# Kernel tuning notes

Hardware: AMD Instinct MI355X
Metric: run time of the kernel (lower is better)

Reference implementation:

```python
import jax, jax.numpy as jnp
import numpy as np
import math

D_MODEL = 1024
N_HEADS = 16
D_K = D_MODEL // N_HEADS
FFN = 4096
B, S = 4, 1024
EPS = 1e-5


def setup_inputs() -> dict:
    key = jax.random.key(0)
    ks = jax.random.split(key, 24)
    sd = 0.02
    def w(k, shape):
        return jax.random.normal(k, shape, dtype=jnp.float32) * sd
    inp = {
        'x': jax.random.normal(ks[0], (B, S, D_MODEL), dtype=jnp.float32),
        'enc': jax.random.normal(ks[1], (B, S, D_MODEL), dtype=jnp.float32),
        'mask': jnp.tril(jnp.ones((S, S), dtype=jnp.int32)),  # causal look-ahead mask
        # stacked per-head projections [H, d_model, d_k], biases [H, d_k]
        'Wq_self': w(ks[2], (N_HEADS, D_MODEL, D_K)), 'bq_self': w(ks[3], (N_HEADS, D_K)),
        'Wk_self': w(ks[4], (N_HEADS, D_MODEL, D_K)), 'bk_self': w(ks[5], (N_HEADS, D_K)),
        'Wv_self': w(ks[6], (N_HEADS, D_MODEL, D_K)), 'bv_self': w(ks[7], (N_HEADS, D_K)),
        'Wq_x': w(ks[8], (N_HEADS, D_MODEL, D_K)), 'bq_x': w(ks[9], (N_HEADS, D_K)),
        'Wk_x': w(ks[10], (N_HEADS, D_MODEL, D_K)), 'bk_x': w(ks[11], (N_HEADS, D_K)),
        'Wv_x': w(ks[12], (N_HEADS, D_MODEL, D_K)), 'bv_x': w(ks[13], (N_HEADS, D_K)),
        # W_O is SHARED between self- and cross-attention (as in the torch code)
        'Wo': w(ks[14], (D_MODEL, D_MODEL)), 'bo': w(ks[15], (D_MODEL,)),
        'W1': w(ks[16], (D_MODEL, FFN)), 'b1': w(ks[17], (FFN,)),
        'W2': w(ks[18], (FFN, D_MODEL)), 'b2': w(ks[19], (D_MODEL,)),
        'g1': jnp.ones((D_MODEL,), jnp.float32), 'be1': jnp.zeros((D_MODEL,), jnp.float32),
        'g2': jnp.ones((D_MODEL,), jnp.float32), 'be2': jnp.zeros((D_MODEL,), jnp.float32),
        'g3': jnp.ones((D_MODEL,), jnp.float32), 'be3': jnp.zeros((D_MODEL,), jnp.float32),
    }
    return inp


def _layernorm(x, g, b):
    mu = jnp.mean(x, axis=-1, keepdims=True)
    d = x - mu
    var = jnp.mean(d * d, axis=-1, keepdims=True)
    return d * jax.lax.rsqrt(var + EPS) * g + b


def _mha(xq, xkv, Wq, bq, Wk, bk, Wv, bv, mask):
    # batched equivalent of the per-head Python loop
    q = jnp.einsum('bsd,hdk->bhsk', xq, Wq) + bq[None, :, None, :]
    k = jnp.einsum('btd,hdk->bhtk', xkv, Wk) + bk[None, :, None, :]
    v = jnp.einsum('btd,hdk->bhtk', xkv, Wv) + bv[None, :, None, :]
    scores = jnp.einsum('bhsk,bhtk->bhst', q, k) / math.sqrt(D_K)
    if mask is not None:
        scores = jnp.where(mask[None, None] == 0, -jnp.inf, scores)
    attn = jax.nn.softmax(scores, axis=-1)
    z = jnp.einsum('bhst,bhtk->bhsk', attn, v)
    # concat heads along last dim (head i occupies slice i, matching torch.cat)
    b_, h_, s_, k_ = z.shape
    return jnp.transpose(z, (0, 2, 1, 3)).reshape(b_, s_, h_ * k_)


def reference(x, enc, mask, Wq_self, bq_self, Wk_self, bk_self, Wv_self, bv_self,
              Wq_x, bq_x, Wk_x, bk_x, Wv_x, bv_x, Wo, bo, W1, b1, W2, b2,
              g1, be1, g2, be2, g3, be3):
    sa = _mha(x, x, Wq_self, bq_self, Wk_self, bk_self, Wv_self, bv_self, mask)
    x1 = _layernorm(x + sa @ Wo + bo, g1, be1)
    ca = _mha(x1, enc, Wq_x, bq_x, Wk_x, bk_x, Wv_x, bv_x, None)
    x2 = _layernorm(x1 + ca @ Wo + bo, g2, be2)
    ffn = jax.nn.relu(x2 @ W1 + b1) @ W2 + b2
    return _layernorm(x2 + ffn, g3, be3)
```

## Files before the change

### kernel.cpp

```cpp
#include <hip/hip_runtime.h>
#include <cstdint>

typedef __bf16 bf16_t;
typedef bf16_t bf16x8 __attribute__((ext_vector_type(8)));
typedef bf16_t bf16x4 __attribute__((ext_vector_type(4)));
typedef float  f32x4  __attribute__((ext_vector_type(4)));

#define DEVI static __device__ __forceinline__

DEVI void async_ld16(const bf16_t* g, bf16_t* l) {
  __builtin_amdgcn_global_load_lds((const __attribute__((address_space(1))) void*)g,
                                   (__attribute__((address_space(3))) void*)l, 16, 0, 0);
}

struct PrepArgs {
  const float *WqS, *WkS, *WvS, *WqX, *WkX, *WvX, *Wo, *W1, *W2, *x, *enc;
  const float *bqS, *bkS, *bvS, *bkX, *bvX;
  bf16_t *WqkvST, *WqXT, *WkvXT, *WoT, *W1T, *W2T, *xb, *encb;
  float *bqkv, *bkvx;
};

__global__ __launch_bounds__(256)
void k_prep(PrepArgs a)
{
  __shared__ float tile[32][33];
  const int blk = blockIdx.x, tid = threadIdx.x;
  const int tx = tid & 31, ty = tid >> 5;

  const float* src = nullptr;
  bf16_t* dst = nullptr;
  int srcLd = 0, dstLd = 0, m0 = 0, n0 = 0;
  bool do_tr = false;

  if (blk < 6144) {
    int j = blk >> 10, q = blk & 1023;
    src = j == 0 ? a.WqS : j == 1 ? a.WkS : j == 2 ? a.WvS : j == 3 ? a.WqX : j == 4 ? a.WkX : a.WvX;
    dst = j == 0 ? a.WqkvST : j == 1 ? a.WqkvST + 1048576 : j == 2 ? a.WqkvST + 2097152
        : j == 3 ? a.WqXT : j == 4 ? a.WkvXT : a.WkvXT + 1048576;
    int batch = q >> 6, rem = q & 63;
    src += (long)batch * 65536; dst += (long)batch * 65536;
    srcLd = 64; dstLd = 1024;
    n0 = (rem & 1) * 32; m0 = (rem >> 1) * 32;
    do_tr = true;
  } else if (blk < 7168) {
    int q = blk - 6144;
    src = a.Wo; dst = a.WoT; srcLd = 1024; dstLd = 1024;
    m0 = (q >> 5) * 32; n0 = (q & 31) * 32; do_tr = true;
  } else if (blk < 11264) {
    int q = blk - 7168;
    src = a.W1; dst = a.W1T; srcLd = 4096; dstLd = 1024;
    m0 = (q >> 7) * 32; n0 = (q & 127) * 32; do_tr = true;
  } else if (blk < 15360) {
    int q = blk - 11264;
    src = a.W2; dst = a.W2T; srcLd = 1024; dstLd = 4096;
    m0 = (q >> 5) * 32; n0 = (q & 31) * 32; do_tr = true;
  } else if (blk < 16384) {
    long base = (long)(blk - 15360) * 4096 + tid * 4;
#pragma unroll
    for (int u = 0; u < 4; u++) {
      float4 v = *(const float4*)(a.x + base + u * 1024);
      bf16x4 o; o[0] = (bf16_t)v.x; o[1] = (bf16_t)v.y; o[2] = (bf16_t)v.z; o[3] = (bf16_t)v.w;
      *(bf16x4*)(a.xb + base + u * 1024) = o;
    }
    return;
  } else if (blk < 17408) {
    long base = (long)(blk - 16384) * 4096 + tid * 4;
#pragma unroll
    for (int u = 0; u < 4; u++) {
      float4 v = *(const float4*)(a.enc + base + u * 1024);
      bf16x4 o; o[0] = (bf16_t)v.x; o[1] = (bf16_t)v.y; o[2] = (bf16_t)v.z; o[3] = (bf16_t)v.w;
      *(bf16x4*)(a.encb + base + u * 1024) = o;
    }
    return;
  } else {
    int gi = (blk - 17408) * 1024 + tid * 4;
#pragma unroll
    for (int j = 0; j < 4; j++) {
      int i = gi + j;
      if (i < 1024)      a.bqkv[i] = a.bqS[i];
      else if (i < 2048) a.bqkv[i] = a.bkS[i - 1024];
      else if (i < 3072) a.bqkv[i] = a.bvS[i - 2048];
      else if (i < 4096) a.bkvx[i - 3072] = a.bkX[i - 3072];
      else if (i < 5120) a.bkvx[i - 3072] = a.bvX[i - 4096];
    }
    return;
  }

  if (do_tr) {
#pragma unroll
    for (int i = 0; i < 4; i++)
      tile[ty + i * 8][tx] = src[(long)(m0 + ty + i * 8) * srcLd + n0 + tx];
    __syncthreads();
#pragma unroll
    for (int i = 0; i < 4; i++)
      dst[(long)(n0 + ty + i * 8) * dstLd + m0 + tx] = (bf16_t)tile[tx][ty + i * 8];
  }
}

template<int OUT_MODE, int RELU>
__global__ __launch_bounds__(256, 2)
void k_gemm(const bf16_t* __restrict__ A, int lda,
            const bf16_t* __restrict__ Bt, int ldb,
            const float* __restrict__ bias,
            bf16_t* __restrict__ C, int ldc,
            bf16_t* __restrict__ p0, bf16_t* __restrict__ p1,
            bf16_t* __restrict__ p2, bf16_t* __restrict__ p3,
            int Ktot, int nx)
{
  __shared__ bf16_t As[2][128 * 32];
  __shared__ bf16_t Bs[2][128 * 32];
  const int tid  = threadIdx.x;
  const int wave = tid >> 6, lane = tid & 63;
  const int quad = lane >> 4, m16 = lane & 15;

  int lin = blockIdx.x;
  int perx = gridDim.x >> 3;
  int t = (lin & 7) * perx + (lin >> 3);
  const int bcol = (t % nx) * 128, brow = (t / nx) * 128;
  const int wr = (wave >> 1) * 64, wc = (wave & 1) * 64;

  const int Kper = Ktot / gridDim.z;
  const int k0 = blockIdx.z * Kper;

  f32x4 acc[4][4];
#pragma unroll
  for (int i = 0; i < 4; i++)
#pragma unroll
    for (int j = 0; j < 4; j++) acc[i][j] = (f32x4){0.f, 0.f, 0.f, 0.f};

  auto stage = [&](int kt, int buf) {
#pragma unroll
    for (int i = 0; i < 2; i++) {
      int rg = wave * 2 + i;
      async_ld16(A  + (long)(brow + rg * 16 + m16) * lda + kt + quad * 8, As[buf] + rg * 512);
      async_ld16(Bt + (long)(bcol + rg * 16 + m16) * ldb + kt + quad * 8, Bs[buf] + rg * 512);
    }
  };

  stage(k0, 0);
  __syncthreads();

  const int nIter = Kper >> 5;
  for (int it = 0; it < nIter; it++) {
    const int cur = it & 1;
    if (it + 1 < nIter) stage(k0 + (it + 1) * 32, cur ^ 1);

    bf16x8 af[4], bfr[4];
#pragma unroll
    for (int tt = 0; tt < 4; tt++) {
      af[tt]  = *(const bf16x8*)(As[cur] + ((wr + tt * 16) >> 4) * 512 + quad * 128 + m16 * 8);
      bfr[tt] = *(const bf16x8*)(Bs[cur] + ((wc + tt * 16) >> 4) * 512 + quad * 128 + m16 * 8);
    }
#pragma unroll
    for (int i = 0; i < 4; i++)
#pragma unroll
      for (int j = 0; j < 4; j++)
        acc[i][j] = __builtin_amdgcn_mfma_f32_16x16x32_bf16(af[i], bfr[j], acc[i][j], 0, 0, 0);

    __syncthreads();
  }

  if (OUT_MODE == 1) {
    bf16_t* P = blockIdx.z == 0 ? p0 : blockIdx.z == 1 ? p1 : blockIdx.z == 2 ? p2 : p3;
#pragma unroll
    for (int i = 0; i < 4; i++)
#pragma unroll
      for (int j = 0; j < 4; j++) {
        int col = bcol + wc + j * 16 + m16;
#pragma unroll
        for (int r = 0; r < 4; r++) {
          int row = brow + wr + i * 16 + quad * 4 + r;
          P[(long)row * ldc + col] = (bf16_t)acc[i][j][r];
        }
      }
  } else {
#pragma unroll
    for (int i = 0; i < 4; i++)
#pragma unroll
      for (int j = 0; j < 4; j++) {
        int col = bcol + wc + j * 16 + m16;
        float bv = bias[col];
#pragma unroll
        for (int r = 0; r < 4; r++) {
          int row = brow + wr + i * 16 + quad * 4 + r;
          float v = acc[i][j][r] + bv;
          if (RELU) v = v > 0.f ? v : 0.f;
          C[(long)row * ldc + col] = (bf16_t)v;
        }
      }
  }
}

__global__ __launch_bounds__(256, 2)
void k_gemm_qkv(const bf16_t* __restrict__ A0, const bf16_t* __restrict__ B0,
                const float* __restrict__ bias0, bf16_t* __restrict__ C0, bf16_t* __restrict__ Vt0,
                const bf16_t* __restrict__ A1, const bf16_t* __restrict__ B1,
                const float* __restrict__ bias1, bf16_t* __restrict__ C1, bf16_t* __restrict__ Vt1)
{
  __shared__ bf16_t As[2][128 * 32];
  __shared__ bf16_t Bs[2][128 * 32];
  const int tid  = threadIdx.x;
  const int wave = tid >> 6, lane = tid & 63;
  const int quad = lane >> 4, m16 = lane & 15;

  int lin = blockIdx.x;
  int perx = gridDim.x >> 3;
  int t = (lin & 7) * perx + (lin >> 3);

  const bf16_t *A, *Bt; const float* bias; bf16_t *C, *Vt;
  int nx, ldc, voff, qthresh, tl;
  if (t < 768) {
    A = A0; Bt = B0; bias = bias0; C = C0; Vt = Vt0;
    nx = 24; ldc = 2048; voff = 2048; qthresh = 1024; tl = t;
  } else {
    A = A1; Bt = B1; bias = bias1; C = C1; Vt = Vt1;
    nx = 16; ldc = 1024; voff = 1024; qthresh = 0; tl = t - 768;
  }
  const int bcol = (tl % nx) * 128, brow = (tl / nx) * 128;
  const int wr = (wave >> 1) * 64, wc = (wave & 1) * 64;

  f32x4 acc[4][4];
#pragma unroll
  for (int i = 0; i < 4; i++)
#pragma unroll
    for (int j = 0; j < 4; j++) acc[i][j] = (f32x4){0.f, 0.f, 0.f, 0.f};

  auto stage = [&](int kt, int buf) {
#pragma unroll
    for (int i = 0; i < 2; i++) {
      int rg = wave * 2 + i;
      async_ld16(A  + (long)(brow + rg * 16 + m16) * 1024 + kt + quad * 8, As[buf] + rg * 512);
      async_ld16(Bt + (long)(bcol + rg * 16 + m16) * 1024 + kt + quad * 8, Bs[buf] + rg * 512);
    }
  };

  stage(0, 0);
  __syncthreads();

  for (int it = 0; it < 32; it++) {
    const int cur = it & 1;
    if (it + 1 < 32) stage((it + 1) * 32, cur ^ 1);

    bf16x8 af[4], bfr[4];
#pragma unroll
    for (int tt = 0; tt < 4; tt++) {
      af[tt]  = *(const bf16x8*)(As[cur] + ((wr + tt * 16) >> 4) * 512 + quad * 128 + m16 * 8);
      bfr[tt] = *(const bf16x8*)(Bs[cur] + ((wc + tt * 16) >> 4) * 512 + quad * 128 + m16 * 8);
    }
#pragma unroll
    for (int i = 0; i < 4; i++)
#pragma unroll
      for (int j = 0; j < 4; j++)
        acc[i][j] = __builtin_amdgcn_mfma_f32_16x16x32_bf16(af[i], bfr[j], acc[i][j], 0, 0, 0);

    __syncthreads();
  }

#pragma unroll
  for (int i = 0; i < 4; i++)
#pragma unroll
    for (int j = 0; j < 4; j++) {
      int col = bcol + wc + j * 16 + m16;
      float bv = bias[col];
      if (col >= voff) {
        int hh = (col - voff) >> 6, dd = col & 63;
        int row0 = brow + wr + i * 16 + quad * 4;
        int bb = row0 >> 10, seq = row0 & 1023;
        bf16x4 pk;
#pragma unroll
        for (int r = 0; r < 4; r++) pk[r] = (bf16_t)(acc[i][j][r] + bv);
        *(bf16x4*)(Vt + (long)(bb * 16 + hh) * 65536 + dd * 1024 + seq) = pk;
      } else {
        float sc = (col < qthresh) ? 0.125f : 1.0f;
#pragma unroll
        for (int r = 0; r < 4; r++) {
          int row = brow + wr + i * 16 + quad * 4 + r;
          C[(long)row * ldc + col] = (bf16_t)((acc[i][j][r] + bv) * sc);
        }
      }
    }
}

template<int LN, int RESID, int OUTF, int OUTB, int QS>
__global__ __launch_bounds__(256)
void k_reduce4(const bf16_t* __restrict__ p0, const bf16_t* __restrict__ p1,
               const bf16_t* __restrict__ p2, const bf16_t* __restrict__ p3,
               const float* __restrict__ bias, const float* __restrict__ resid,
               const float* __restrict__ gamma, const float* __restrict__ beta,
               float* __restrict__ outf, bf16_t* __restrict__ outb)
{
  constexpr int D = 1024;
  __shared__ float red[8];
  int row = blockIdx.x, tid = threadIdx.x;
  long off = (long)row * D + tid * 4;
  bf16x4 a0 = *(const bf16x4*)(p0 + off);
  bf16x4 a1 = *(const bf16x4*)(p1 + off);
  bf16x4 a2 = *(const bf16x4*)(p2 + off);
  bf16x4 a3 = *(const bf16x4*)(p3 + off);
  float4 bb4 = *(const float4*)(bias + tid * 4);
  float4 v;
  v.x = (float)a0[0] + (float)a1[0] + (float)a2[0] + (float)a3[0] + bb4.x;
  v.y = (float)a0[1] + (float)a1[1] + (float)a2[1] + (float)a3[1] + bb4.y;
  v.z = (float)a0[2] + (float)a1[2] + (float)a2[2] + (float)a3[2] + bb4.z;
  v.w = (float)a0[3] + (float)a1[3] + (float)a2[3] + (float)a3[3] + bb4.w;
  if (RESID) {
    float4 q = *(const float4*)(resid + off);
    v.x += q.x; v.y += q.y; v.z += q.z; v.w += q.w;
  }
  float4 y = v;
  if (LN) {
    float s  = v.x + v.y + v.z + v.w;
    float sq = v.x * v.x + v.y * v.y + v.z * v.z + v.w * v.w;
#pragma unroll
    for (int o = 1; o < 64; o <<= 1) {
      s  += __shfl_xor(s, o, 64);
      sq += __shfl_xor(sq, o, 64);
    }
    int wave = tid >> 6, lane = tid & 63;
    if (lane == 0) { red[wave * 2] = s; red[wave * 2 + 1] = sq; }
    __syncthreads();
    float ts = red[0] + red[2] + red[4] + red[6];
    float tq = red[1] + red[3] + red[5] + red[7];
    float mu = ts * (1.f / D);
    float var = tq * (1.f / D) - mu * mu;
    float rstd = rsqrtf(var + 1e-5f);
    float4 g  = *(const float4*)(gamma + tid * 4);
    float4 be = *(const float4*)(beta + tid * 4);
    y.x = (v.x - mu) * rstd * g.x + be.x;
    y.y = (v.y - mu) * rstd * g.y + be.y;
    y.z = (v.z - mu) * rstd * g.z + be.z;
    y.w = (v.w - mu) * rstd * g.w + be.w;
  }
  if (OUTF) *(float4*)(outf + off) = y;
  if (OUTB) {
    if (QS) { y.x *= 0.125f; y.y *= 0.125f; y.z *= 0.125f; y.w *= 0.125f; }
    bf16x4 o;
    o[0] = (bf16_t)y.x; o[1] = (bf16_t)y.y; o[2] = (bf16_t)y.z; o[3] = (bf16_t)y.w;
    *(bf16x4*)(outb + off) = o;
  }
}

template<int CAUSAL>
__global__ __launch_bounds__(256, 2)
void k_attn(const bf16_t* __restrict__ Q, int ldq,
            const bf16_t* __restrict__ Kp, int ldk,
            const bf16_t* __restrict__ Vt,
            bf16_t* __restrict__ O)
{
  constexpr int S = 1024;
  __shared__ bf16_t Kls[2][4096];
  __shared__ bf16_t Vls[2][4096];
  __shared__ bf16_t Pls[4][32 * 72];

  const int tid = threadIdx.x;
  const int wave = tid >> 6, lane = tid & 63;
  const int quad = lane >> 4, m16 = lane & 15;
  const int qt = blockIdx.x, bh = blockIdx.y, b = bh >> 4, h = bh & 15;
  const int qbase = qt * 128 + wave * 32;

  bf16x8 qf[2][2];
#pragma unroll
  for (int rh = 0; rh < 2; rh++) {
    const bf16_t* qp = Q + (long)(b * S + qbase + rh * 16 + m16) * ldq + h * 64 + quad * 8;
    qf[rh][0] = *(const bf16x8*)qp;
    qf[rh][1] = *(const bf16x8*)(qp + 32);
  }

  f32x4 o_acc[2][4];
#pragma unroll
  for (int rh = 0; rh < 2; rh++)
#pragma unroll
    for (int t = 0; t < 4; t++) o_acc[rh][t] = (f32x4){0.f, 0.f, 0.f, 0.f};
  float rsum[2][4];
#pragma unroll
  for (int rh = 0; rh < 2; rh++)
#pragma unroll
    for (int r = 0; r < 4; r++) rsum[rh][r] = 0.f;

  auto stage = [&](int c, int buf) {
#pragma unroll
    for (int i = 0; i < 2; i++) {
      int t2 = wave * 2 + i;
      int rg = t2 & 3, ph = t2 >> 2;
      async_ld16(Kp + (long)(b * S + c * 64 + rg * 16 + m16) * ldk + h * 64 + ph * 32 + quad * 8,
                 Kls[buf] + t2 * 512);
      async_ld16(Vt + (long)bh * 65536 + (rg * 16 + m16) * 1024 + c * 64 + ph * 32 + quad * 8,
                 Vls[buf] + t2 * 512);
    }
  };

  const int nch = CAUSAL ? (2 * qt + 2) : 16;
  stage(0, 0);

  for (int c = 0; c < nch; c++) {
    __syncthreads();
    const int cur = c & 1;
    if (c + 1 < nch) stage(c + 1, cur ^ 1);

    f32x4 s[2][4];
#pragma unroll
    for (int t = 0; t < 4; t++) {
      bf16x8 k0 = *(const bf16x8*)(Kls[cur] + (0 * 4 + t) * 512 + quad * 128 + m16 * 8);
      bf16x8 k1 = *(const bf16x8*)(Kls[cur] + (1 * 4 + t) * 512 + quad * 128 + m16 * 8);
#pragma unroll
      for (int rh = 0; rh < 2; rh++) {
        f32x4 z = (f32x4){0.f, 0.f, 0.f, 0.f};
        z = __builtin_amdgcn_mfma_f32_16x16x32_bf16(qf[rh][0], k0, z, 0, 0, 0);
        z = __builtin_amdgcn_mfma_f32_16x16x32_bf16(qf[rh][1], k1, z, 0, 0, 0);
        s[rh][t] = z;
      }
    }

    bf16_t* pw = Pls[wave];
#pragma unroll
    for (int rh = 0; rh < 2; rh++)
#pragma unroll
      for (int r = 0; r < 4; r++) {
        int qg = qbase + rh * 16 + quad * 4 + r;
#pragma unroll
        for (int t = 0; t < 4; t++) {
          float v = s[rh][t][r];
          float p;
          if (CAUSAL) {
            int kvg = c * 64 + t * 16 + m16;
            p = (kvg <= qg) ? __expf(v) : 0.f;
          } else {
            p = __expf(v);
          }
          rsum[rh][r] += p;
          pw[(rh * 16 + quad * 4 + r) * 72 + t * 16 + m16] = (bf16_t)p;
        }
      }

    bf16x8 pf[2][2];
#pragma unroll
    for (int rh = 0; rh < 2; rh++)
#pragma unroll
      for (int kvh = 0; kvh < 2; kvh++)
        pf[rh][kvh] = *(const bf16x8*)(pw + (rh * 16 + m16) * 72 + kvh * 32 + quad * 8);
#pragma unroll
    for (int t = 0; t < 4; t++) {
      bf16x8 v0 = *(const bf16x8*)(Vls[cur] + (0 * 4 + t) * 512 + quad * 128 + m16 * 8);
      bf16x8 v1 = *(const bf16x8*)(Vls[cur] + (1 * 4 + t) * 512 + quad * 128 + m16 * 8);
#pragma unroll
      for (int rh = 0; rh < 2; rh++) {
        o_acc[rh][t] = __builtin_amdgcn_mfma_f32_16x16x32_bf16(pf[rh][0], v0, o_acc[rh][t], 0, 0, 0);
        o_acc[rh][t] = __builtin_amdgcn_mfma_f32_16x16x32_bf16(pf[rh][1], v1, o_acc[rh][t], 0, 0, 0);
      }
    }
  }

#pragma unroll
  for (int rh = 0; rh < 2; rh++)
#pragma unroll
    for (int r = 0; r < 4; r++) {
      float v = rsum[rh][r];
      v += __shfl_xor(v, 1, 64);
      v += __shfl_xor(v, 2, 64);
      v += __shfl_xor(v, 4, 64);
      v += __shfl_xor(v, 8, 64);
      rsum[rh][r] = 1.f / v;
    }
#pragma unroll
  for (int rh = 0; rh < 2; rh++)
#pragma unroll
    for (int t = 0; t < 4; t++)
#pragma unroll
      for (int r = 0; r < 4; r++) {
        int row = b * S + qbase + rh * 16 + quad * 4 + r;
        int col = h * 64 + t * 16 + m16;
        O[(long)row * 1024 + col] = (bf16_t)(o_acc[rh][t][r] * rsum[rh][r]);
      }
}

extern "C" void kernel_launch(void* const* d_in, const int* in_sizes, int n_in,
                              void* d_out, int out_size, void* d_ws, size_t ws_size,
                              hipStream_t stream)
{
  const float* x   = (const float*)d_in[0];
  const float* enc = (const float*)d_in[1];
  const float* WqS = (const float*)d_in[3];
  const float* bqS = (const float*)d_in[4];
  const float* WkS = (const float*)d_in[5];
  const float* bkS = (const float*)d_in[6];
  const float* WvS = (const float*)d_in[7];
  const float* bvS = (const float*)d_in[8];
  const float* WqX = (const float*)d_in[9];
  const float* bqX = (const float*)d_in[10];
  const float* WkX = (const float*)d_in[11];
  const float* bkX = (const float*)d_in[12];
  const float* WvX = (const float*)d_in[13];
  const float* bvX = (const float*)d_in[14];
  const float* Wo  = (const float*)d_in[15];
  const float* bo  = (const float*)d_in[16];
  const float* W1  = (const float*)d_in[17];
  const float* b1  = (const float*)d_in[18];
  const float* W2  = (const float*)d_in[19];
  const float* b2  = (const float*)d_in[20];
  const float* g1  = (const float*)d_in[21];
  const float* be1 = (const float*)d_in[22];
  const float* g2  = (const float*)d_in[23];
  const float* be2 = (const float*)d_in[24];
  const float* g3  = (const float*)d_in[25];
  const float* be3 = (const float*)d_in[26];

  char* ws = (char*)d_ws;
  const long MBy = 1048576;
  bf16_t* WqkvST = (bf16_t*)(ws + 0 * MBy);
  bf16_t* WqXT   = (bf16_t*)(ws + 6 * MBy);
  bf16_t* WkvXT  = (bf16_t*)(ws + 8 * MBy);
  bf16_t* WoT    = (bf16_t*)(ws + 12 * MBy);
  bf16_t* W1T    = (bf16_t*)(ws + 14 * MBy);
  bf16_t* W2T    = (bf16_t*)(ws + 22 * MBy);
  float*  bqkvS  = (float*)(ws + 30 * MBy);
  float*  bkvX   = (float*)(ws + 30 * MBy + 16384);
  bf16_t* xb     = (bf16_t*)(ws + 31 * MBy);
  bf16_t* Qx     = xb;
  bf16_t* encb   = (bf16_t*)(ws + 39 * MBy);
  float*  x1f    = (float*)(ws + 47 * MBy);
  bf16_t* x1b    = (bf16_t*)(ws + 63 * MBy);
  bf16_t* Z      = (bf16_t*)(ws + 71 * MBy);
  bf16_t* QK     = (bf16_t*)(ws + 79 * MBy);
  bf16_t* Kenc   = (bf16_t*)(ws + 95 * MBy);
  bf16_t* VtS    = (bf16_t*)(ws + 103 * MBy);
  bf16_t* VtX    = (bf16_t*)(ws + 111 * MBy);
  bf16_t* pa0 = (bf16_t*)(ws + 79 * MBy);
  bf16_t* pa1 = (bf16_t*)(ws + 87 * MBy);
  bf16_t* pa2 = (bf16_t*)(ws + 103 * MBy);
  bf16_t* pa3 = (bf16_t*)(ws + 119 * MBy);
  bf16_t* Hbuf = (bf16_t*)(ws + 79 * MBy);
  bf16_t* pf0 = (bf16_t*)(ws + 0 * MBy);
  bf16_t* pf1 = (bf16_t*)(ws + 31 * MBy);
  bf16_t* pf2 = (bf16_t*)(ws + 39 * MBy);
  bf16_t* pf3 = (bf16_t*)(ws + 63 * MBy);

  dim3 tb(256);

  PrepArgs pa;
  pa.WqS = WqS; pa.WkS = WkS; pa.WvS = WvS; pa.WqX = WqX; pa.WkX = WkX; pa.WvX = WvX;
  pa.Wo = Wo; pa.W1 = W1; pa.W2 = W2; pa.x = x; pa.enc = enc;
  pa.bqS = bqS; pa.bkS = bkS; pa.bvS = bvS; pa.bkX = bkX; pa.bvX = bvX;
  pa.WqkvST = WqkvST; pa.WqXT = WqXT; pa.WkvXT = WkvXT; pa.WoT = WoT;
  pa.W1T = W1T; pa.W2T = W2T; pa.xb = xb; pa.encb = encb;
  pa.bqkv = bqkvS; pa.bkvx = bkvX;
  k_prep<<<dim3(17413), tb, 0, stream>>>(pa);

  k_gemm_qkv<<<dim3(1280), tb, 0, stream>>>(
      xb, WqkvST, bqkvS, QK, VtS,
      encb, WkvXT, bkvX, Kenc, VtX);

  k_attn<1><<<dim3(8, 64), tb, 0, stream>>>(QK, 2048, QK + 1024, 2048, VtS, Z);
  k_gemm<1, 0><<<dim3(256, 1, 4), tb, 0, stream>>>(
      Z, 1024, WoT, 1024, nullptr, nullptr, 1024, pa0, pa1, pa2, pa3, 1024, 8);
  k_reduce4<1, 1, 1, 1, 0><<<dim3(4096), tb, 0, stream>>>(
      pa0, pa1, pa2, pa3, bo, x, g1, be1, x1f, x1b);

  k_gemm<1, 0><<<dim3(256, 1, 4), tb, 0, stream>>>(
      x1b, 1024, WqXT, 1024, nullptr, nullptr, 1024, pa0, pa1, pa2, pa3, 1024, 8);
  k_reduce4<0, 0, 0, 1, 1><<<dim3(4096), tb, 0, stream>>>(
      pa0, pa1, pa2, pa3, bqX, nullptr, nullptr, nullptr, nullptr, Qx);
  k_attn<0><<<dim3(8, 64), tb, 0, stream>>>(Qx, 1024, Kenc, 1024, VtX, Z);
  k_gemm<1, 0><<<dim3(256, 1, 4), tb, 0, stream>>>(
      Z, 1024, WoT, 1024, nullptr, nullptr, 1024, pa0, pa1, pa2, pa3, 1024, 8);
  k_reduce4<1, 1, 1, 1, 0><<<dim3(4096), tb, 0, stream>>>(
      pa0, pa1, pa2, pa3, bo, x1f, g2, be2, x1f, x1b);

  k_gemm<0, 1><<<dim3(1024), tb, 0, stream>>>(
      x1b, 1024, W1T, 1024, b1, Hbuf, 4096, nullptr, nullptr, nullptr, nullptr, 1024, 32);
  k_gemm<1, 0><<<dim3(256, 1, 4), tb, 0, stream>>>(
      Hbuf, 4096, W2T, 4096, nullptr, nullptr, 1024, pf0, pf1, pf2, pf3, 4096, 8);
  k_reduce4<1, 1, 1, 0, 0><<<dim3(4096), tb, 0, stream>>>(
      pf0, pf1, pf2, pf3, b2, x1f, g3, be3, (float*)d_out, nullptr);
}
```

Measured before the change: 603.8 us.

## Load GEMM fragments directly from global into registers, dropping LDS staging

Replaces the LDS double-buffered async staging in the GEMM kernels with a shared register double-buffered core. Each lane loads its MFMA fragments straight from global memory, which removes the shared memory and the barriers, and occupancy is raised to 3 blocks per SM. The cost is that waves which previously shared tile data through LDS now each fetch it separately. That roughly doubles L2 traffic and uses strided, less coalesced 16-byte loads per row.

```diff
diff --git a/kernel.cpp b/kernel.cpp
--- a/kernel.cpp
+++ b/kernel.cpp
@@ -97,18 +97,54 @@
   }
 }
 
-template<int OUT_MODE, int RELU>
-__global__ __launch_bounds__(256, 2)
+template<int NITER>
+DEVI void gemm_core(const bf16_t* __restrict__ A, int lda,
+                    const bf16_t* __restrict__ Bt, int ldb,
+                    int brow, int bcol, int k0, int wr, int wc,
+                    int quad, int m16, f32x4 (&acc)[4][4])
+{
+  int aOff[4], bOff[4];
+#pragma unroll
+  for (int i = 0; i < 4; i++) {
+    aOff[i] = (brow + wr + i * 16 + m16) * lda + k0 + quad * 8;
+    bOff[i] = (bcol + wc + i * 16 + m16) * ldb + k0 + quad * 8;
+  }
+
+  bf16x8 aR[2][4], bR[2][4];
+#pragma unroll
+  for (int i = 0; i < 4; i++) {
+    aR[0][i] = *(const bf16x8*)(A + (long)aOff[i]);
+    bR[0][i] = *(const bf16x8*)(Bt + (long)bOff[i]);
+  }
+
+#pragma unroll
+  for (int t = 0; t < NITER; t++) {
+    const int cur = t & 1;
+    if (t + 1 < NITER) {
+#pragma unroll
+      for (int i = 0; i < 4; i++) {
+        aR[cur ^ 1][i] = *(const bf16x8*)(A + (long)aOff[i] + (t + 1) * 32);
+        bR[cur ^ 1][i] = *(const bf16x8*)(Bt + (long)bOff[i] + (t + 1) * 32);
+      }
+    }
+#pragma unroll
+    for (int i = 0; i < 4; i++)
+#pragma unroll
+      for (int j = 0; j < 4; j++)
+        acc[i][j] = __builtin_amdgcn_mfma_f32_16x16x32_bf16(aR[cur][i], bR[cur][j], acc[i][j], 0, 0, 0);
+  }
+}
+
+template<int OUT_MODE, int RELU, int NITER>
+__global__ __launch_bounds__(256, 3)
 void k_gemm(const bf16_t* __restrict__ A, int lda,
             const bf16_t* __restrict__ Bt, int ldb,
             const float* __restrict__ bias,
             bf16_t* __restrict__ C, int ldc,
             bf16_t* __restrict__ p0, bf16_t* __restrict__ p1,
             bf16_t* __restrict__ p2, bf16_t* __restrict__ p3,
-            int Ktot, int nx)
-{
-  __shared__ bf16_t As[2][128 * 32];
-  __shared__ bf16_t Bs[2][128 * 32];
+            int nx)
+{
   const int tid  = threadIdx.x;
   const int wave = tid >> 6, lane = tid & 63;
   const int quad = lane >> 4, m16 = lane & 15;
@@ -118,9 +154,7 @@
   int t = (lin & 7) * perx + (lin >> 3);
   const int bcol = (t % nx) * 128, brow = (t / nx) * 128;
   const int wr = (wave >> 1) * 64, wc = (wave & 1) * 64;
-
-  const int Kper = Ktot / gridDim.z;
-  const int k0 = blockIdx.z * Kper;
+  const int k0 = blockIdx.z * (NITER * 32);
 
   f32x4 acc[4][4];
 #pragma unroll
@@ -128,37 +162,7 @@
 #pragma unroll
     for (int j = 0; j < 4; j++) acc[i][j] = (f32x4){0.f, 0.f, 0.f, 0.f};
 
-  auto stage = [&](int kt, int buf) {
-#pragma unroll
-    for (int i = 0; i < 2; i++) {
-      int rg = wave * 2 + i;
-      async_ld16(A  + (long)(brow + rg * 16 + m16) * lda + kt + quad * 8, As[buf] + rg * 512);
-      async_ld16(Bt + (long)(bcol + rg * 16 + m16) * ldb + kt + quad * 8, Bs[buf] + rg * 512);
-    }
-  };
-
-  stage(k0, 0);
-  __syncthreads();
-
-  const int nIter = Kper >> 5;
-  for (int it = 0; it < nIter; it++) {
-    const int cur = it & 1;
-    if (it + 1 < nIter) stage(k0 + (it + 1) * 32, cur ^ 1);
-
-    bf16x8 af[4], bfr[4];
-#pragma unroll
-    for (int tt = 0; tt < 4; tt++) {
-      af[tt]  = *(const bf16x8*)(As[cur] + ((wr + tt * 16) >> 4) * 512 + quad * 128 + m16 * 8);
-      bfr[tt] = *(const bf16x8*)(Bs[cur] + ((wc + tt * 16) >> 4) * 512 + quad * 128 + m16 * 8);
-    }
-#pragma unroll
-    for (int i = 0; i < 4; i++)
-#pragma unroll
-      for (int j = 0; j < 4; j++)
-        acc[i][j] = __builtin_amdgcn_mfma_f32_16x16x32_bf16(af[i], bfr[j], acc[i][j], 0, 0, 0);
-
-    __syncthreads();
-  }
+  gemm_core<NITER>(A, lda, Bt, ldb, brow, bcol, k0, wr, wc, quad, m16, acc);
 
   if (OUT_MODE == 1) {
     bf16_t* P = blockIdx.z == 0 ? p0 : blockIdx.z == 1 ? p1 : blockIdx.z == 2 ? p2 : p3;
@@ -191,14 +195,12 @@
   }
 }
 
-__global__ __launch_bounds__(256, 2)
+__global__ __launch_bounds__(256, 3)
 void k_gemm_qkv(const bf16_t* __restrict__ A0, const bf16_t* __restrict__ B0,
                 const float* __restrict__ bias0, bf16_t* __restrict__ C0, bf16_t* __restrict__ Vt0,
                 const bf16_t* __restrict__ A1, const bf16_t* __restrict__ B1,
                 const float* __restrict__ bias1, bf16_t* __restrict__ C1, bf16_t* __restrict__ Vt1)
 {
-  __shared__ bf16_t As[2][128 * 32];
-  __shared__ bf16_t Bs[2][128 * 32];
   const int tid  = threadIdx.x;
   const int wave = tid >> 6, lane = tid & 63;
   const int quad = lane >> 4, m16 = lane & 15;
@@ -225,36 +227,7 @@
 #pragma unroll
     for (int j = 0; j < 4; j++) acc[i][j] = (f32x4){0.f, 0.f, 0.f, 0.f};
 
-  auto stage = [&](int kt, int buf) {
-#pragma unroll
-    for (int i = 0; i < 2; i++) {
-      int rg = wave * 2 + i;
-      async_ld16(A  + (long)(brow + rg * 16 + m16) * 1024 + kt + quad * 8, As[buf] + rg * 512);
-      async_ld16(Bt + (long)(bcol + rg * 16 + m16) * 1024 + kt + quad * 8, Bs[buf] + rg * 512);
-    }
-  };
-
-  stage(0, 0);
-  __syncthreads();
-
-  for (int it = 0; it < 32; it++) {
-    const int cur = it & 1;
-    if (it + 1 < 32) stage((it + 1) * 32, cur ^ 1);
-
-    bf16x8 af[4], bfr[4];
-#pragma unroll
-    for (int tt = 0; tt < 4; tt++) {
-      af[tt]  = *(const bf16x8*)(As[cur] + ((wr + tt * 16) >> 4) * 512 + quad * 128 + m16 * 8);
-      bfr[tt] = *(const bf16x8*)(Bs[cur] + ((wc + tt * 16) >> 4) * 512 + quad * 128 + m16 * 8);
-    }
-#pragma unroll
-    for (int i = 0; i < 4; i++)
-#pragma unroll
-      for (int j = 0; j < 4; j++)
-        acc[i][j] = __builtin_amdgcn_mfma_f32_16x16x32_bf16(af[i], bfr[j], acc[i][j], 0, 0, 0);
-
-    __syncthreads();
-  }
+  gemm_core<32>(A, 1024, Bt, 1024, brow, bcol, 0, wr, wc, quad, m16, acc);
 
 #pragma unroll
   for (int i = 0; i < 4; i++)
@@ -550,25 +523,25 @@
       encb, WkvXT, bkvX, Kenc, VtX);
 
   k_attn<1><<<dim3(8, 64), tb, 0, stream>>>(QK, 2048, QK + 1024, 2048, VtS, Z);
-  k_gemm<1, 0><<<dim3(256, 1, 4), tb, 0, stream>>>(
-      Z, 1024, WoT, 1024, nullptr, nullptr, 1024, pa0, pa1, pa2, pa3, 1024, 8);
+  k_gemm<1, 0, 8><<<dim3(256, 1, 4), tb, 0, stream>>>(
+      Z, 1024, WoT, 1024, nullptr, nullptr, 1024, pa0, pa1, pa2, pa3, 8);
   k_reduce4<1, 1, 1, 1, 0><<<dim3(4096), tb, 0, stream>>>(
       pa0, pa1, pa2, pa3, bo, x, g1, be1, x1f, x1b);
 
-  k_gemm<1, 0><<<dim3(256, 1, 4), tb, 0, stream>>>(
-      x1b, 1024, WqXT, 1024, nullptr, nullptr, 1024, pa0, pa1, pa2, pa3, 1024, 8);
+  k_gemm<1, 0, 8><<<dim3(256, 1, 4), tb, 0, stream>>>(
+      x1b, 1024, WqXT, 1024, nullptr, nullptr, 1024, pa0, pa1, pa2, pa3, 8);
   k_reduce4<0, 0, 0, 1, 1><<<dim3(4096), tb, 0, stream>>>(
       pa0, pa1, pa2, pa3, bqX, nullptr, nullptr, nullptr, nullptr, Qx);
   k_attn<0><<<dim3(8, 64), tb, 0, stream>>>(Qx, 1024, Kenc, 1024, VtX, Z);
-  k_gemm<1, 0><<<dim3(256, 1, 4), tb, 0, stream>>>(
-      Z, 1024, WoT, 1024, nullptr, nullptr, 1024, pa0, pa1, pa2, pa3, 1024, 8);
+  k_gemm<1, 0, 8><<<dim3(256, 1, 4), tb, 0, stream>>>(
+      Z, 1024, WoT, 1024, nullptr, nullptr, 1024, pa0, pa1, pa2, pa3, 8);
   k_reduce4<1, 1, 1, 1, 0><<<dim3(4096), tb, 0, stream>>>(
       pa0, pa1, pa2, pa3, bo, x1f, g2, be2, x1f, x1b);
 
-  k_gemm<0, 1><<<dim3(1024), tb, 0, stream>>>(
-      x1b, 1024, W1T, 1024, b1, Hbuf, 4096, nullptr, nullptr, nullptr, nullptr, 1024, 32);
-  k_gemm<1, 0><<<dim3(256, 1, 4), tb, 0, stream>>>(
-      Hbuf, 4096, W2T, 4096, nullptr, nullptr, 1024, pf0, pf1, pf2, pf3, 4096, 8);
+  k_gemm<0, 1, 32><<<dim3(1024), tb, 0, stream>>>(
+      x1b, 1024, W1T, 1024, b1, Hbuf, 4096, nullptr, nullptr, nullptr, nullptr, 32);
+  k_gemm<1, 0, 32><<<dim3(256, 1, 4), tb, 0, stream>>>(
+      Hbuf, 4096, W2T, 4096, nullptr, nullptr, 1024, pf0, pf1, pf2, pf3, 8);
   k_reduce4<1, 1, 1, 0, 0><<<dim3(4096), tb, 0, stream>>>(
       pf0, pf1, pf2, pf3, b2, x1f, g3, be3, (float*)d_out, nullptr);
 }
```

Measured after the change: 847.7 us. 40.4% more time.
